# Performance work log

Hardware: AMD Instinct MI355X
Metric: run time of the kernel (lower is better)

Reference implementation:

```python
import jax, jax.numpy as jnp
import numpy as np

D_MODEL = 1024
NUM_HEADS = 16
D_K = D_MODEL // NUM_HEADS  # 64
THETA = 10000.0
B, S = 2, 2048


def _rope(x, cos, sin):
    # x: [b, h, s, d]; cos/sin: [s, d//2] (broadcast over b, h)
    x1 = x[..., 0::2]
    x2 = x[..., 1::2]
    y1 = x1 * cos - x2 * sin
    y2 = x1 * sin + x2 * cos
    # interleave back: stack on last dim then flatten pairs
    return jnp.stack([y1, y2], axis=-1).reshape(x.shape)


def setup_inputs() -> dict:
    key = jax.random.key(0)
    ks = jax.random.split(key, 5)
    scale = 1.0 / np.sqrt(D_MODEL)
    return {
        "x": jax.random.normal(ks[0], (B, S, D_MODEL), dtype=jnp.float32),
        "token_positions": jnp.arange(S, dtype=jnp.int32),
        "Wq": jax.random.normal(ks[1], (D_MODEL, D_MODEL), dtype=jnp.float32) * scale,
        "Wk": jax.random.normal(ks[2], (D_MODEL, D_MODEL), dtype=jnp.float32) * scale,
        "Wv": jax.random.normal(ks[3], (D_MODEL, D_MODEL), dtype=jnp.float32) * scale,
        "Wo": jax.random.normal(ks[4], (D_MODEL, D_MODEL), dtype=jnp.float32) * scale,
    }


def reference(x, token_positions, Wq, Wk, Wv, Wo):
    b, s, _ = x.shape
    # torch nn.Linear semantics (no bias in this repo's Linear): y = x @ W.T
    q = jnp.einsum("bsd,od->bso", x, Wq)
    k = jnp.einsum("bsd,od->bso", x, Wk)
    v = jnp.einsum("bsd,od->bso", x, Wv)
    # split heads: b s (h d) -> b h s d
    def split(t):
        return t.reshape(b, s, NUM_HEADS, D_K).transpose(0, 2, 1, 3)
    q, k, v = split(q), split(k), split(v)

    # RoPE tables
    inv_freq = 1.0 / (THETA ** (jnp.arange(0, D_K, 2, dtype=jnp.float32) / D_K))  # [d/2]
    freqs = token_positions.astype(jnp.float32)[:, None] * inv_freq[None, :]      # [s, d/2]
    cos, sin = jnp.cos(freqs), jnp.sin(freqs)
    q = _rope(q, cos, sin)
    k = _rope(k, cos, sin)

    scale = D_K ** (-0.5)
    scores = jnp.einsum("bhqd,bhkd->bhqk", q, k) * scale  # [b,h,s,s]
    causal = jnp.tril(jnp.ones((s, s), dtype=bool))
    scores = jnp.where(causal, scores, -jnp.inf)
    attn = jax.nn.softmax(scores, axis=-1)
    out = jnp.einsum("bhqk,bhkd->bhqd", attn, v)
    out = out.transpose(0, 2, 1, 3).reshape(b, s, D_MODEL)  # b h s d -> b s (h d)
    return jnp.einsum("bsd,od->bso", out, Wo)
```

## Files before the change

kernel.cpp:

```cpp
#include <hip/hip_runtime.h>
#include <hip/hip_bf16.h>
#include <math.h>

#define SS 2048

typedef __attribute__((ext_vector_type(8))) __bf16 bf16x8;
typedef __attribute__((ext_vector_type(4))) float f32x4;
typedef __attribute__((ext_vector_type(16))) float f32x16;
typedef __attribute__((ext_vector_type(4))) unsigned int u32x4;
typedef __attribute__((ext_vector_type(4))) unsigned short u16x4;

__device__ __forceinline__ f32x4 mfma16(bf16x8 a, bf16x8 b, f32x4 c) {
  return __builtin_amdgcn_mfma_f32_16x16x32_bf16(a, b, c, 0, 0, 0);
}
__device__ __forceinline__ f32x16 mfma32(bf16x8 a, bf16x8 b, f32x16 c) {
  return __builtin_amdgcn_mfma_f32_32x32x16_bf16(a, b, c, 0, 0, 0);
}

__device__ __forceinline__ void gld_lds16(const void* g, void* l) {
  __builtin_amdgcn_global_load_lds(
      (__attribute__((address_space(1))) void*)(g),
      (__attribute__((address_space(3))) void*)(l), 16, 0, 0);
}

#if __has_builtin(__builtin_amdgcn_exp2f)
#define EXP2F(x) __builtin_amdgcn_exp2f(x)
#else
#define EXP2F(x) __expf(0.69314718056f * (x))
#endif

__device__ __forceinline__ unsigned int cvtpk_bf16(float lo, float hi) {
  unsigned int r;
  asm("v_cvt_pk_bf16_f32 %0, %1, %2" : "=v"(r) : "v"(lo), "v"(hi));
  return r;
}
__device__ __forceinline__ void swap32(unsigned int& x, unsigned int& y) {
  asm("v_permlane32_swap_b32 %0, %1" : "+v"(x), "+v"(y));
}
__device__ __forceinline__ unsigned short bfu(float v) {
  __bf16 h = (__bf16)v;
  return __builtin_bit_cast(unsigned short, h);
}

__global__ void prep_kernel(const float* __restrict__ x, const float* __restrict__ Wq,
                            const float* __restrict__ Wk, const float* __restrict__ Wv,
                            const float* __restrict__ Wo, const int* __restrict__ pos,
                            __bf16* __restrict__ xb, __bf16* __restrict__ Wb,
                            float2* __restrict__ tab) {
  const int bid = blockIdx.x, tid = threadIdx.x;
  if (bid >= 4096) {
    int i = (bid - 4096) * 256 + tid;
    int s = i >> 5, j = i & 31;
    float p = (float)pos[s];
    float inv = exp2f((float)j * -0.41524101186098283f);
    float f = p * inv;
    float sn, cs;
    sincosf(f, &sn, &cs);
    tab[i] = make_float2(cs, sn);
    return;
  }
  const float* s;
  __bf16* d;
  size_t base;
  if (bid < 2048) { s = x; d = xb; base = bid; }
  else {
    int seg = (bid - 2048) >> 9;
    s = (seg == 0) ? Wq : (seg == 1) ? Wk : (seg == 2) ? Wv : Wo;
    d = Wb + (size_t)seg * 1024 * 1024;
    base = (bid - 2048) & 511;
  }
  size_t i = (base * 256 + tid) * 8;
  float4 a = *reinterpret_cast<const float4*>(s + i);
  float4 b = *reinterpret_cast<const float4*>(s + i + 4);
  bf16x8 o;
  o[0] = (__bf16)a.x; o[1] = (__bf16)a.y; o[2] = (__bf16)a.z; o[3] = (__bf16)a.w;
  o[4] = (__bf16)b.x; o[5] = (__bf16)b.y; o[6] = (__bf16)b.z; o[7] = (__bf16)b.w;
  *reinterpret_cast<bf16x8*>(d + i) = o;
}

__global__ __launch_bounds__(512, 1) void gemm256_kernel(
    const __bf16* __restrict__ A, const __bf16* __restrict__ Bw,
    __bf16* __restrict__ C, __bf16* __restrict__ Vt,
    const float2* __restrict__ tab) {
  const int K = 1024, N = 3072, nk = 32;
  __shared__ __align__(16) __bf16 sm[65536];
  __bf16* lsA = sm;
  __bf16* lsB = sm + 32768;

  const int tid = threadIdx.x;
  const int lane = tid & 63;
  const int wave = tid >> 6;
  const int wr = wave >> 2, wc = wave & 3;

  const int xcd = blockIdx.x & 7;
  const int ii = blockIdx.x >> 3;
  const int m0 = (2 * xcd + (ii & 1)) * 256;
  const int n0 = (ii >> 1) * 256;

  const f32x4 fzero = {0.f, 0.f, 0.f, 0.f};
  f32x4 acc[8][4];
#pragma unroll
  for (int f = 0; f < 8; ++f)
#pragma unroll
    for (int g = 0; g < 4; ++g) acc[f][g] = fzero;

  const int srow = tid >> 2, schunk = tid & 3;
  const int ssc = schunk ^ ((srow >> 1) & 3);
  const __bf16* gA = A + (size_t)(m0 + srow) * K + ssc * 8;
  const __bf16* gB = Bw + (size_t)(n0 + srow) * K + ssc * 8;
  const size_t half128 = (size_t)128 * K;

#define STAGE256(kt_)                                              \
  do {                                                             \
    const int kc_ = (kt_) & 3;                                     \
    const __bf16* ga_ = gA + (size_t)(kt_) * 32;                   \
    const __bf16* gb_ = gB + (size_t)(kt_) * 32;                   \
    gld_lds16(ga_, lsA + kc_ * 8192 + tid * 8);                    \
    gld_lds16(ga_ + half128, lsA + kc_ * 8192 + 4096 + tid * 8);   \
    gld_lds16(gb_, lsB + kc_ * 8192 + tid * 8);                    \
    gld_lds16(gb_ + half128, lsB + kc_ * 8192 + 4096 + tid * 8);   \
  } while (0)

  STAGE256(0);
  STAGE256(1);

  const int lrow = lane & 15, hi = lane >> 4;

#pragma unroll 1
  for (int kt = 0; kt < nk; ++kt) {
    const int ks = (kt & 3) * 8192;
    if (kt + 2 < nk) {
      STAGE256(kt + 2);
      asm volatile("s_waitcnt vmcnt(8)" ::: "memory");
    } else if (kt == nk - 2) {
      asm volatile("s_waitcnt vmcnt(4)" ::: "memory");
    } else {
      asm volatile("s_waitcnt vmcnt(0)" ::: "memory");
    }
    __builtin_amdgcn_s_barrier();

    bf16x8 bfr[4];
#pragma unroll
    for (int g = 0; g < 4; ++g) {
      const int r = wc * 64 + g * 16 + lrow;
      bfr[g] = *reinterpret_cast<const bf16x8*>(
          lsB + ks + r * 32 + ((hi ^ ((r >> 1) & 3)) * 8));
    }
    bf16x8 af[4];
#pragma unroll
    for (int f = 0; f < 4; ++f) {
      const int r = wr * 128 + f * 16 + lrow;
      af[f] = *reinterpret_cast<const bf16x8*>(
          lsA + ks + r * 32 + ((hi ^ ((r >> 1) & 3)) * 8));
    }
    __builtin_amdgcn_s_setprio(1);
#pragma unroll
    for (int f = 0; f < 4; ++f)
#pragma unroll
      for (int g = 0; g < 4; ++g) acc[f][g] = mfma16(af[f], bfr[g], acc[f][g]);
    __builtin_amdgcn_s_setprio(0);
#pragma unroll
    for (int f = 0; f < 4; ++f) {
      const int r = wr * 128 + (f + 4) * 16 + lrow;
      af[f] = *reinterpret_cast<const bf16x8*>(
          lsA + ks + r * 32 + ((hi ^ ((r >> 1) & 3)) * 8));
    }
    __builtin_amdgcn_s_setprio(1);
#pragma unroll
    for (int f = 0; f < 4; ++f)
#pragma unroll
      for (int g = 0; g < 4; ++g) acc[f + 4][g] = mfma16(af[f], bfr[g], acc[f + 4][g]);
    __builtin_amdgcn_s_setprio(0);
  }
#undef STAGE256

  const int crow = (lane >> 4) * 4, ccol = lane & 15;
  if (n0 < 2048) {
    const int par = ccol & 1;
#pragma unroll
    for (int f = 0; f < 8; ++f) {
#pragma unroll
      for (int t = 0; t < 4; ++t) {
        const int r = m0 + wr * 128 + f * 16 + crow + t;
        const int s = r & (SS - 1);
#pragma unroll
        for (int g = 0; g < 4; ++g) {
          const int c = n0 + wc * 64 + g * 16 + ccol;
          const int jj = (c >> 1) & 31;
          float2 cs = tab[(s << 5) | jj];
          float v = acc[f][g][t];
          float o = __shfl_xor(v, 1);
          float y = par ? fmaf(o, cs.y, v * cs.x) : fmaf(v, cs.x, -o * cs.y);
          C[(size_t)r * N + c] = (__bf16)y;
        }
      }
    }
  } else {
#pragma unroll
    for (int f = 0; f < 8; ++f) {
      const int r0 = m0 + wr * 128 + f * 16 + crow;
      const int bb = r0 >> 11, s0 = r0 & (SS - 1);
#pragma unroll
      for (int g = 0; g < 4; ++g) {
        const int c = n0 - 2048 + wc * 64 + g * 16 + ccol;
        const int hh = c >> 6, dd = c & 63;
        u16x4 pk;
#pragma unroll
        for (int t = 0; t < 4; ++t) pk[t] = bfu(acc[f][g][t]);
        *reinterpret_cast<u16x4*>(Vt + ((size_t)(bb * 16 + hh) * 64 + dd) * SS + s0) = pk;
      }
    }
  }
}

template <typename OutT>
__global__ __launch_bounds__(256) void gemm_bt_kernel(
    const __bf16* __restrict__ A, const __bf16* __restrict__ Bw,
    OutT* __restrict__ C, int MT, int N, int K) {
  __shared__ __align__(16) __bf16 lA[2][128 * 32];
  __shared__ __align__(16) __bf16 lB[2][128 * 32];
  const int tid = threadIdx.x;
  const int lane = tid & 63;
  const int wave = tid >> 6;
  const int wr = wave >> 1, wc = wave & 1;

  const int cpx = (int)gridDim.x >> 3;
  const int flat = blockIdx.x;
  const int wg = (flat & 7) * cpx + (flat >> 3);
  const int MB = MT >> 3;
  const int NT = (int)gridDim.x / MT;
  const int band = wg / (MB * NT);
  const int inner = wg % (MB * NT);
  const int m0 = (band * MB + (inner % MB)) * 128;
  const int n0 = (inner / MB) * 128;

  const f32x4 fzero = {0.f, 0.f, 0.f, 0.f};
  f32x4 acc[4][4];
#pragma unroll
  for (int i = 0; i < 4; ++i)
#pragma unroll
    for (int j = 0; j < 4; ++j) acc[i][j] = fzero;

  const int srow = tid >> 2, scol = (tid & 3) * 8;
  const __bf16* gA = A + (size_t)(m0 + srow) * K + scol;
  const __bf16* gB = Bw + (size_t)(n0 + srow) * K + scol;
  const size_t half = (size_t)64 * K;
  const int lrow = lane & 15, lk8 = (lane >> 4) * 8;

  gld_lds16(gA, &lA[0][tid * 8]);
  gld_lds16(gA + half, &lA[0][tid * 8 + 2048]);
  gld_lds16(gB, &lB[0][tid * 8]);
  gld_lds16(gB + half, &lB[0][tid * 8 + 2048]);
  __syncthreads();

  const int nk = K >> 5;
  for (int t = 0; t < nk; ++t) {
    const int buf = t & 1;
    if (t + 1 < nk) {
      const int kt = (t + 1) * 32;
      gld_lds16(gA + kt, &lA[buf ^ 1][tid * 8]);
      gld_lds16(gA + kt + half, &lA[buf ^ 1][tid * 8 + 2048]);
      gld_lds16(gB + kt, &lB[buf ^ 1][tid * 8]);
      gld_lds16(gB + kt + half, &lB[buf ^ 1][tid * 8 + 2048]);
    }
    bf16x8 af[4], bfr[4];
#pragma unroll
    for (int i = 0; i < 4; ++i)
      af[i] = *reinterpret_cast<const bf16x8*>(&lA[buf][(wr * 64 + i * 16 + lrow) * 32 + lk8]);
#pragma unroll
    for (int j = 0; j < 4; ++j)
      bfr[j] = *reinterpret_cast<const bf16x8*>(&lB[buf][(wc * 64 + j * 16 + lrow) * 32 + lk8]);
    __builtin_amdgcn_s_setprio(1);
#pragma unroll
    for (int i = 0; i < 4; ++i)
#pragma unroll
      for (int j = 0; j < 4; ++j) acc[i][j] = mfma16(af[i], bfr[j], acc[i][j]);
    __builtin_amdgcn_s_setprio(0);
    __syncthreads();
  }

  const int crow = (lane >> 4) * 4, ccol = lane & 15;
#pragma unroll
  for (int i = 0; i < 4; ++i) {
#pragma unroll
    for (int j = 0; j < 4; ++j) {
      int r = m0 + wr * 64 + i * 16 + crow;
      int c = n0 + wc * 64 + j * 16 + ccol;
#pragma unroll
      for (int t = 0; t < 4; ++t) C[(size_t)(r + t) * N + c] = (OutT)acc[i][j][t];
    }
  }
}

#define CEXP 0.18033688011112042f
#define SHIFT_B 16.0f

#define EXPSUM(S0, S1, L)                                                   \
  {                                                                         \
    float a0_ = 0.f, a1_ = 0.f, a2_ = 0.f, a3_ = 0.f;                       \
    _Pragma("unroll") for (int r = 0; r < 16; r += 4) {                     \
      S0[r] = EXP2F(fmaf(S0[r], CEXP, -SHIFT_B)); a0_ += S0[r];             \
      S0[r + 1] = EXP2F(fmaf(S0[r + 1], CEXP, -SHIFT_B)); a1_ += S0[r + 1]; \
      S0[r + 2] = EXP2F(fmaf(S0[r + 2], CEXP, -SHIFT_B)); a2_ += S0[r + 2]; \
      S0[r + 3] = EXP2F(fmaf(S0[r + 3], CEXP, -SHIFT_B)); a3_ += S0[r + 3]; \
    }                                                                       \
    _Pragma("unroll") for (int r = 0; r < 16; r += 4) {                     \
      S1[r] = EXP2F(fmaf(S1[r], CEXP, -SHIFT_B)); a0_ += S1[r];             \
      S1[r + 1] = EXP2F(fmaf(S1[r + 1], CEXP, -SHIFT_B)); a1_ += S1[r + 1]; \
      S1[r + 2] = EXP2F(fmaf(S1[r + 2], CEXP, -SHIFT_B)); a2_ += S1[r + 2]; \
      S1[r + 3] = EXP2F(fmaf(S1[r + 3], CEXP, -SHIFT_B)); a3_ += S1[r + 3]; \
    }                                                                       \
    float rs_ = (a0_ + a1_) + (a2_ + a3_);                                  \
    rs_ += __shfl_xor(rs_, 32);                                             \
    L += rs_;                                                               \
  }

__global__ __launch_bounds__(128) void attn_kernel(const __bf16* __restrict__ qkv,
                                                   const __bf16* __restrict__ Vt,
                                                   __bf16* __restrict__ AO) {
  const int bid = blockIdx.x;
  const int x = bid & 7, t7 = bid >> 3;
  const int low = t7 & 7, phi = (t7 >> 3) & 3, g = t7 >> 5;
  const int p = phi * 8 + x;
  const int b = p >> 4, h = p & 15;
  const int qt = (g == 0) ? low : (g == 1) ? 31 - low : (g == 2) ? 15 - low : 16 + low;

  const int tid = threadIdx.x;
  const int wave = tid >> 6, lane = tid & 63;
  const int q32 = lane & 31, hi = lane >> 5;
  const int qw0 = qt * 64 + wave * 32;
  const int q = qw0 + q32;

  __shared__ __align__(16) __bf16 smem[16384];
  __bf16* lK0 = smem;
  __bf16* lV0 = smem + 8192;

  bf16x8 qb[4];
  {
    const __bf16* qr = qkv + (size_t)(b * SS + q) * 3072 + h * 64;
#pragma unroll
    for (int slot = 0; slot < 4; ++slot)
      qb[slot] = *reinterpret_cast<const bf16x8*>(qr + slot * 16 + hi * 8);
  }

  const __bf16* kbase = qkv + (size_t)(b * SS) * 3072 + 1024 + h * 64;
  const __bf16* vbase = Vt + (size_t)((b * 16 + h) * 64) * SS;

  const int srow = tid >> 3, scg = tid & 7;
  const int ssc = 8 * (scg ^ (srow & 7));
  const __bf16* kG0 = kbase + (size_t)srow * 3072 + ssc;
  const __bf16* vG0 = vbase + (size_t)srow * SS + ssc;

#define STAGE(buf_, kt_)                                                      \
  do {                                                                        \
    const __bf16* kG = kG0 + (size_t)(kt_)*64 * 3072;                         \
    const __bf16* vG = vG0 + (size_t)(kt_)*64;                                \
    _Pragma("unroll") for (int u = 0; u < 4; ++u) {                           \
      gld_lds16(kG + (size_t)u * 16 * 3072, lK0 + (buf_)*4096 + tid * 8 + u * 1024); \
      gld_lds16(vG + (size_t)u * 16 * SS, lV0 + (buf_)*4096 + tid * 8 + u * 1024);   \
    }                                                                         \
  } while (0)

  f32x16 o0 = {0,0,0,0,0,0,0,0,0,0,0,0,0,0,0,0};
  f32x16 o1 = {0,0,0,0,0,0,0,0,0,0,0,0,0,0,0,0};
  float lsum = 0.f;

  const int nkt = qt + 1;
  STAGE(0, 0);
  __syncthreads();

  for (int kt = 0; kt < nkt; ++kt) {
    const int buf = kt & 1;
    const int kvb = kt * 64;
    if (kt + 1 < nkt) STAGE(buf ^ 1, kt + 1);

    const __bf16* lk = lK0 + buf * 4096;
    const __bf16* lv = lV0 + buf * 4096;

    f32x16 s0 = {0,0,0,0,0,0,0,0,0,0,0,0,0,0,0,0};
    f32x16 s1 = {0,0,0,0,0,0,0,0,0,0,0,0,0,0,0,0};
    __builtin_amdgcn_s_setprio(1);
#pragma unroll
    for (int slot = 0; slot < 4; ++slot) {
      const int swz = 8 * ((slot * 2 + hi) ^ (q32 & 7));
      bf16x8 k0 = *reinterpret_cast<const bf16x8*>(lk + q32 * 64 + swz);
      bf16x8 k1 = *reinterpret_cast<const bf16x8*>(lk + (32 + q32) * 64 + swz);
      s0 = mfma32(k0, qb[slot], s0);
      s1 = mfma32(k1, qb[slot], s1);
    }
    __builtin_amdgcn_s_setprio(0);

    if (kt == qt) {
#pragma unroll
      for (int r = 0; r < 16; ++r) {
        const int rowc = (r & 3) + 8 * (r >> 2) + 4 * hi;
        if (kvb + rowc > q) s0[r] = -INFINITY;
        if (kvb + 32 + rowc > q) s1[r] = -INFINITY;
      }
    }

    EXPSUM(s0, s1, lsum)

    bf16x8 pb[4];
    {
      unsigned int A = cvtpk_bf16(s0[0], s0[1]), B2 = cvtpk_bf16(s0[2], s0[3]);
      unsigned int C2 = cvtpk_bf16(s0[4], s0[5]), D2 = cvtpk_bf16(s0[6], s0[7]);
      swap32(A, C2); swap32(B2, D2);
      u32x4 t0 = {A, B2, C2, D2};
      pb[0] = __builtin_bit_cast(bf16x8, t0);
      unsigned int E = cvtpk_bf16(s0[8], s0[9]), F = cvtpk_bf16(s0[10], s0[11]);
      unsigned int G = cvtpk_bf16(s0[12], s0[13]), H = cvtpk_bf16(s0[14], s0[15]);
      swap32(E, G); swap32(F, H);
      u32x4 t1 = {E, F, G, H};
      pb[1] = __builtin_bit_cast(bf16x8, t1);
      unsigned int A3 = cvtpk_bf16(s1[0], s1[1]), B3 = cvtpk_bf16(s1[2], s1[3]);
      unsigned int C3 = cvtpk_bf16(s1[4], s1[5]), D3 = cvtpk_bf16(s1[6], s1[7]);
      swap32(A3, C3); swap32(B3, D3);
      u32x4 t2 = {A3, B3, C3, D3};
      pb[2] = __builtin_bit_cast(bf16x8, t2);
      unsigned int E3 = cvtpk_bf16(s1[8], s1[9]), F3 = cvtpk_bf16(s1[10], s1[11]);
      unsigned int G3 = cvtpk_bf16(s1[12], s1[13]), H3 = cvtpk_bf16(s1[14], s1[15]);
      swap32(E3, G3); swap32(F3, H3);
      u32x4 t3 = {E3, F3, G3, H3};
      pb[3] = __builtin_bit_cast(bf16x8, t3);
    }

    __builtin_amdgcn_s_setprio(1);
#pragma unroll
    for (int slot = 0; slot < 4; ++slot) {
      const int swz = 8 * ((slot * 2 + hi) ^ (q32 & 7));
      bf16x8 v0 = *reinterpret_cast<const bf16x8*>(lv + q32 * 64 + swz);
      bf16x8 v1 = *reinterpret_cast<const bf16x8*>(lv + (32 + q32) * 64 + swz);
      o0 = mfma32(v0, pb[slot], o0);
      o1 = mfma32(v1, pb[slot], o1);
    }
    __builtin_amdgcn_s_setprio(0);

    __syncthreads();
  }

  const float inv = 1.0f / lsum;
  __bf16* ol = smem + wave * 2304;
#pragma unroll
  for (int r = 0; r < 16; ++r) {
    const int d = (r & 3) + 8 * (r >> 2) + 4 * hi;
    ol[q32 * 72 + d] = (__bf16)(o0[r] * inv);
    ol[q32 * 72 + 32 + d] = (__bf16)(o1[r] * inv);
  }
#pragma unroll
  for (int pass = 0; pass < 4; ++pass) {
    const int idx = pass * 64 + lane;
    const int row = idx >> 3, colc = idx & 7;
    bf16x8 v = *reinterpret_cast<const bf16x8*>(ol + row * 72 + colc * 8);
    *reinterpret_cast<bf16x8*>(
        AO + (size_t)(b * SS + qt * 64 + wave * 32 + row) * 1024 + h * 64 + colc * 8) = v;
  }
#undef STAGE
}

extern "C" void kernel_launch(void* const* d_in, const int* in_sizes, int n_in,
                              void* d_out, int out_size, void* d_ws, size_t ws_size,
                              hipStream_t stream) {
  const float* x  = (const float*)d_in[0];
  const int* pos  = (const int*)d_in[1];
  const float* Wq = (const float*)d_in[2];
  const float* Wk = (const float*)d_in[3];
  const float* Wv = (const float*)d_in[4];
  const float* Wo = (const float*)d_in[5];

  __bf16* xb  = (__bf16*)d_ws;
  __bf16* Wb  = xb + (size_t)4096 * 1024;
  __bf16* qkv = Wb + (size_t)4096 * 1024;
  __bf16* Vt  = qkv + (size_t)4096 * 3072;
  __bf16* ao  = Vt + (size_t)2048 * 2048;
  float2* tab = (float2*)(ao + (size_t)4096 * 1024);

  prep_kernel<<<4352, 256, 0, stream>>>(x, Wq, Wk, Wv, Wo, pos, xb, Wb, tab);
  gemm256_kernel<<<192, 512, 0, stream>>>(xb, Wb, qkv, Vt, tab);
  attn_kernel<<<1024, 128, 0, stream>>>(qkv, Vt, ao);
  gemm_bt_kernel<float><<<256, 256, 0, stream>>>(
      ao, Wb + (size_t)3 * 1024 * 1024, (float*)d_out, 32, 1024, 1024);
}
```

Baseline: 113.5 us.

## Retile QKV GEMM to 256x192 for full CU coverage and rewrite output GEMM

The QKV projection GEMM now uses 256x192 tiles, so it launches 256 workgroups instead of 192 and fills all 256 CUs. Only six of the eight waves load the B tile, and the wait counts are adjusted per wave. The epilogue now decides per 16-column group whether to apply RoPE or write the transposed V. The output projection is replaced by a 512-thread kernel with a 4-stage swizzled LDS pipeline, XCD-aware tile mapping and a single barrier per k-step. The cost is a smaller N tile per workgroup, which lowers the compute per byte loaded.

```diff
diff --git a/kernel.cpp b/kernel.cpp
--- a/kernel.cpp
+++ b/kernel.cpp
@@ -83,7 +83,7 @@
     __bf16* __restrict__ C, __bf16* __restrict__ Vt,
     const float2* __restrict__ tab) {
   const int K = 1024, N = 3072, nk = 32;
-  __shared__ __align__(16) __bf16 sm[65536];
+  __shared__ __align__(16) __bf16 sm[57344];
   __bf16* lsA = sm;
   __bf16* lsB = sm + 32768;
 
@@ -91,34 +91,38 @@
   const int lane = tid & 63;
   const int wave = tid >> 6;
   const int wr = wave >> 2, wc = wave & 3;
+  const bool lowW = wave < 6;
 
   const int xcd = blockIdx.x & 7;
   const int ii = blockIdx.x >> 3;
   const int m0 = (2 * xcd + (ii & 1)) * 256;
-  const int n0 = (ii >> 1) * 256;
+  const int n0 = (ii >> 1) * 192;
 
   const f32x4 fzero = {0.f, 0.f, 0.f, 0.f};
-  f32x4 acc[8][4];
+  f32x4 acc[8][3];
 #pragma unroll
   for (int f = 0; f < 8; ++f)
 #pragma unroll
-    for (int g = 0; g < 4; ++g) acc[f][g] = fzero;
-
-  const int srow = tid >> 2, schunk = tid & 3;
-  const int ssc = schunk ^ ((srow >> 1) & 3);
-  const __bf16* gA = A + (size_t)(m0 + srow) * K + ssc * 8;
-  const __bf16* gB = Bw + (size_t)(n0 + srow) * K + ssc * 8;
-  const size_t half128 = (size_t)128 * K;
-
-#define STAGE256(kt_)                                              \
-  do {                                                             \
-    const int kc_ = (kt_) & 3;                                     \
-    const __bf16* ga_ = gA + (size_t)(kt_) * 32;                   \
-    const __bf16* gb_ = gB + (size_t)(kt_) * 32;                   \
-    gld_lds16(ga_, lsA + kc_ * 8192 + tid * 8);                    \
-    gld_lds16(ga_ + half128, lsA + kc_ * 8192 + 4096 + tid * 8);   \
-    gld_lds16(gb_, lsB + kc_ * 8192 + tid * 8);                    \
-    gld_lds16(gb_ + half128, lsB + kc_ * 8192 + 4096 + tid * 8);   \
+    for (int g = 0; g < 3; ++g) acc[f][g] = fzero;
+
+  const int arow0 = tid >> 2, ac = tid & 3;
+  const __bf16* gA0 = A + (size_t)(m0 + arow0) * K + 8 * (ac ^ ((arow0 >> 1) & 3));
+  const __bf16* gA1 = A + (size_t)(m0 + 128 + arow0) * K + 8 * (ac ^ (((arow0 + 128) >> 1) & 3));
+  const int bid0 = tid, bid1 = tid + 384;
+  const int br0 = bid0 >> 2, br1 = bid1 >> 2;
+  const __bf16* gB0 = Bw + (size_t)(n0 + br0) * K + 8 * ((bid0 & 3) ^ ((br0 >> 1) & 3));
+  const __bf16* gB1 = Bw + (size_t)(n0 + br1) * K + 8 * ((bid1 & 3) ^ ((br1 >> 1) & 3));
+
+#define STAGE256(kt_)                                                \
+  do {                                                               \
+    const int kc_ = (kt_) & 3;                                       \
+    const int ko_ = (kt_) * 32;                                      \
+    gld_lds16(gA0 + ko_, lsA + kc_ * 8192 + tid * 8);                \
+    gld_lds16(gA1 + ko_, lsA + kc_ * 8192 + 4096 + tid * 8);         \
+    if (lowW) {                                                      \
+      gld_lds16(gB0 + ko_, lsB + kc_ * 6144 + tid * 8);              \
+      gld_lds16(gB1 + ko_, lsB + kc_ * 6144 + 3072 + tid * 8);       \
+    }                                                                \
   } while (0)
 
   STAGE256(0);
@@ -128,82 +132,81 @@
 
 #pragma unroll 1
   for (int kt = 0; kt < nk; ++kt) {
-    const int ks = (kt & 3) * 8192;
+    const int ksA = (kt & 3) * 8192, ksB = (kt & 3) * 6144;
     if (kt + 2 < nk) {
       STAGE256(kt + 2);
-      asm volatile("s_waitcnt vmcnt(8)" ::: "memory");
+      if (lowW) asm volatile("s_waitcnt vmcnt(8)" ::: "memory");
+      else      asm volatile("s_waitcnt vmcnt(4)" ::: "memory");
     } else if (kt == nk - 2) {
-      asm volatile("s_waitcnt vmcnt(4)" ::: "memory");
+      if (lowW) asm volatile("s_waitcnt vmcnt(4)" ::: "memory");
+      else      asm volatile("s_waitcnt vmcnt(2)" ::: "memory");
     } else {
       asm volatile("s_waitcnt vmcnt(0)" ::: "memory");
     }
     __builtin_amdgcn_s_barrier();
 
-    bf16x8 bfr[4];
-#pragma unroll
-    for (int g = 0; g < 4; ++g) {
-      const int r = wc * 64 + g * 16 + lrow;
+    bf16x8 bfr[3];
+#pragma unroll
+    for (int g = 0; g < 3; ++g) {
+      const int r = wc * 48 + g * 16 + lrow;
       bfr[g] = *reinterpret_cast<const bf16x8*>(
-          lsB + ks + r * 32 + ((hi ^ ((r >> 1) & 3)) * 8));
+          lsB + ksB + r * 32 + ((hi ^ ((r >> 1) & 3)) * 8));
     }
     bf16x8 af[4];
 #pragma unroll
     for (int f = 0; f < 4; ++f) {
       const int r = wr * 128 + f * 16 + lrow;
       af[f] = *reinterpret_cast<const bf16x8*>(
-          lsA + ks + r * 32 + ((hi ^ ((r >> 1) & 3)) * 8));
+          lsA + ksA + r * 32 + ((hi ^ ((r >> 1) & 3)) * 8));
     }
     __builtin_amdgcn_s_setprio(1);
 #pragma unroll
     for (int f = 0; f < 4; ++f)
 #pragma unroll
-      for (int g = 0; g < 4; ++g) acc[f][g] = mfma16(af[f], bfr[g], acc[f][g]);
+      for (int g = 0; g < 3; ++g) acc[f][g] = mfma16(af[f], bfr[g], acc[f][g]);
     __builtin_amdgcn_s_setprio(0);
 #pragma unroll
     for (int f = 0; f < 4; ++f) {
       const int r = wr * 128 + (f + 4) * 16 + lrow;
       af[f] = *reinterpret_cast<const bf16x8*>(
-          lsA + ks + r * 32 + ((hi ^ ((r >> 1) & 3)) * 8));
+          lsA + ksA + r * 32 + ((hi ^ ((r >> 1) & 3)) * 8));
     }
     __builtin_amdgcn_s_setprio(1);
 #pragma unroll
     for (int f = 0; f < 4; ++f)
 #pragma unroll
-      for (int g = 0; g < 4; ++g) acc[f + 4][g] = mfma16(af[f], bfr[g], acc[f + 4][g]);
+      for (int g = 0; g < 3; ++g) acc[f + 4][g] = mfma16(af[f], bfr[g], acc[f + 4][g]);
     __builtin_amdgcn_s_setprio(0);
   }
 #undef STAGE256
 
   const int crow = (lane >> 4) * 4, ccol = lane & 15;
-  if (n0 < 2048) {
-    const int par = ccol & 1;
-#pragma unroll
-    for (int f = 0; f < 8; ++f) {
-#pragma unroll
-      for (int t = 0; t < 4; ++t) {
-        const int r = m0 + wr * 128 + f * 16 + crow + t;
-        const int s = r & (SS - 1);
-#pragma unroll
-        for (int g = 0; g < 4; ++g) {
-          const int c = n0 + wc * 64 + g * 16 + ccol;
-          const int jj = (c >> 1) & 31;
+  const int par = ccol & 1;
+#pragma unroll
+  for (int g = 0; g < 3; ++g) {
+    const int cb = n0 + wc * 48 + g * 16;
+    if (cb < 2048) {
+      const int jj = ((cb + ccol) >> 1) & 31;
+#pragma unroll
+      for (int f = 0; f < 8; ++f) {
+#pragma unroll
+        for (int t = 0; t < 4; ++t) {
+          const int r = m0 + wr * 128 + f * 16 + crow + t;
+          const int s = r & (SS - 1);
           float2 cs = tab[(s << 5) | jj];
           float v = acc[f][g][t];
           float o = __shfl_xor(v, 1);
           float y = par ? fmaf(o, cs.y, v * cs.x) : fmaf(v, cs.x, -o * cs.y);
-          C[(size_t)r * N + c] = (__bf16)y;
+          C[(size_t)r * N + cb + ccol] = (__bf16)y;
         }
       }
-    }
-  } else {
-#pragma unroll
-    for (int f = 0; f < 8; ++f) {
-      const int r0 = m0 + wr * 128 + f * 16 + crow;
-      const int bb = r0 >> 11, s0 = r0 & (SS - 1);
-#pragma unroll
-      for (int g = 0; g < 4; ++g) {
-        const int c = n0 - 2048 + wc * 64 + g * 16 + ccol;
-        const int hh = c >> 6, dd = c & 63;
+    } else {
+      const int c = cb - 2048 + ccol;
+      const int hh = c >> 6, dd = c & 63;
+#pragma unroll
+      for (int f = 0; f < 8; ++f) {
+        const int r0 = m0 + wr * 128 + f * 16 + crow;
+        const int bb = r0 >> 11, s0 = r0 & (SS - 1);
         u16x4 pk;
 #pragma unroll
         for (int t = 0; t < 4; ++t) pk[t] = bfu(acc[f][g][t]);
@@ -213,81 +216,92 @@
   }
 }
 
-template <typename OutT>
-__global__ __launch_bounds__(256) void gemm_bt_kernel(
+__global__ __launch_bounds__(512, 1) void gemm_out_kernel(
     const __bf16* __restrict__ A, const __bf16* __restrict__ Bw,
-    OutT* __restrict__ C, int MT, int N, int K) {
-  __shared__ __align__(16) __bf16 lA[2][128 * 32];
-  __shared__ __align__(16) __bf16 lB[2][128 * 32];
+    float* __restrict__ C) {
+  const int K = 1024, N = 1024, nk = 32;
+  __shared__ __align__(16) __bf16 sm[32768];
+  __bf16* lsA = sm;
+  __bf16* lsB = sm + 16384;
+
   const int tid = threadIdx.x;
   const int lane = tid & 63;
   const int wave = tid >> 6;
-  const int wr = wave >> 1, wc = wave & 1;
-
-  const int cpx = (int)gridDim.x >> 3;
-  const int flat = blockIdx.x;
-  const int wg = (flat & 7) * cpx + (flat >> 3);
-  const int MB = MT >> 3;
-  const int NT = (int)gridDim.x / MT;
-  const int band = wg / (MB * NT);
-  const int inner = wg % (MB * NT);
-  const int m0 = (band * MB + (inner % MB)) * 128;
-  const int n0 = (inner / MB) * 128;
+  const int wr = wave >> 2, wc = wave & 3;
+
+  const int xcd = blockIdx.x & 7;
+  const int ii = blockIdx.x >> 3;
+  const int m0 = (4 * xcd + (ii & 3)) * 128;
+  const int n0 = (ii >> 2) * 128;
 
   const f32x4 fzero = {0.f, 0.f, 0.f, 0.f};
-  f32x4 acc[4][4];
-#pragma unroll
-  for (int i = 0; i < 4; ++i)
-#pragma unroll
-    for (int j = 0; j < 4; ++j) acc[i][j] = fzero;
-
-  const int srow = tid >> 2, scol = (tid & 3) * 8;
-  const __bf16* gA = A + (size_t)(m0 + srow) * K + scol;
-  const __bf16* gB = Bw + (size_t)(n0 + srow) * K + scol;
-  const size_t half = (size_t)64 * K;
-  const int lrow = lane & 15, lk8 = (lane >> 4) * 8;
-
-  gld_lds16(gA, &lA[0][tid * 8]);
-  gld_lds16(gA + half, &lA[0][tid * 8 + 2048]);
-  gld_lds16(gB, &lB[0][tid * 8]);
-  gld_lds16(gB + half, &lB[0][tid * 8 + 2048]);
-  __syncthreads();
-
-  const int nk = K >> 5;
-  for (int t = 0; t < nk; ++t) {
-    const int buf = t & 1;
-    if (t + 1 < nk) {
-      const int kt = (t + 1) * 32;
-      gld_lds16(gA + kt, &lA[buf ^ 1][tid * 8]);
-      gld_lds16(gA + kt + half, &lA[buf ^ 1][tid * 8 + 2048]);
-      gld_lds16(gB + kt, &lB[buf ^ 1][tid * 8]);
-      gld_lds16(gB + kt + half, &lB[buf ^ 1][tid * 8 + 2048]);
-    }
-    bf16x8 af[4], bfr[4];
-#pragma unroll
-    for (int i = 0; i < 4; ++i)
-      af[i] = *reinterpret_cast<const bf16x8*>(&lA[buf][(wr * 64 + i * 16 + lrow) * 32 + lk8]);
-#pragma unroll
-    for (int j = 0; j < 4; ++j)
-      bfr[j] = *reinterpret_cast<const bf16x8*>(&lB[buf][(wc * 64 + j * 16 + lrow) * 32 + lk8]);
+  f32x4 acc[4][2];
+#pragma unroll
+  for (int f = 0; f < 4; ++f)
+#pragma unroll
+    for (int g = 0; g < 2; ++g) acc[f][g] = fzero;
+
+  const int srow = tid >> 2, sc = tid & 3;
+  const int ssc = 8 * (sc ^ ((srow >> 1) & 3));
+  const __bf16* gA = A + (size_t)(m0 + srow) * K + ssc;
+  const __bf16* gB = Bw + (size_t)(n0 + srow) * K + ssc;
+
+#define STAGEO(kt_)                                        \
+  do {                                                     \
+    const int kc_ = (kt_) & 3;                             \
+    gld_lds16(gA + (kt_) * 32, lsA + kc_ * 4096 + tid * 8);\
+    gld_lds16(gB + (kt_) * 32, lsB + kc_ * 4096 + tid * 8);\
+  } while (0)
+
+  STAGEO(0);
+  STAGEO(1);
+
+  const int lrow = lane & 15, hi = lane >> 4;
+
+#pragma unroll 1
+  for (int kt = 0; kt < nk; ++kt) {
+    const int ks = (kt & 3) * 4096;
+    if (kt + 2 < nk) {
+      STAGEO(kt + 2);
+      asm volatile("s_waitcnt vmcnt(4)" ::: "memory");
+    } else if (kt == nk - 2) {
+      asm volatile("s_waitcnt vmcnt(2)" ::: "memory");
+    } else {
+      asm volatile("s_waitcnt vmcnt(0)" ::: "memory");
+    }
+    __builtin_amdgcn_s_barrier();
+
+    bf16x8 bfr[2], af[4];
+#pragma unroll
+    for (int g = 0; g < 2; ++g) {
+      const int r = wc * 32 + g * 16 + lrow;
+      bfr[g] = *reinterpret_cast<const bf16x8*>(
+          lsB + ks + r * 32 + ((hi ^ ((r >> 1) & 3)) * 8));
+    }
+#pragma unroll
+    for (int f = 0; f < 4; ++f) {
+      const int r = wr * 64 + f * 16 + lrow;
+      af[f] = *reinterpret_cast<const bf16x8*>(
+          lsA + ks + r * 32 + ((hi ^ ((r >> 1) & 3)) * 8));
+    }
     __builtin_amdgcn_s_setprio(1);
 #pragma unroll
-    for (int i = 0; i < 4; ++i)
-#pragma unroll
-      for (int j = 0; j < 4; ++j) acc[i][j] = mfma16(af[i], bfr[j], acc[i][j]);
+    for (int f = 0; f < 4; ++f)
+#pragma unroll
+      for (int g = 0; g < 2; ++g) acc[f][g] = mfma16(af[f], bfr[g], acc[f][g]);
     __builtin_amdgcn_s_setprio(0);
-    __syncthreads();
-  }
+  }
+#undef STAGEO
 
   const int crow = (lane >> 4) * 4, ccol = lane & 15;
 #pragma unroll
-  for (int i = 0; i < 4; ++i) {
-#pragma unroll
-    for (int j = 0; j < 4; ++j) {
-      int r = m0 + wr * 64 + i * 16 + crow;
-      int c = n0 + wc * 64 + j * 16 + ccol;
-#pragma unroll
-      for (int t = 0; t < 4; ++t) C[(size_t)(r + t) * N + c] = (OutT)acc[i][j][t];
+  for (int f = 0; f < 4; ++f) {
+#pragma unroll
+    for (int g = 0; g < 2; ++g) {
+      int r = m0 + wr * 64 + f * 16 + crow;
+      int c = n0 + wc * 32 + g * 16 + ccol;
+#pragma unroll
+      for (int t = 0; t < 4; ++t) C[(size_t)(r + t) * N + c] = acc[f][g][t];
     }
   }
 }
@@ -476,8 +490,7 @@
   float2* tab = (float2*)(ao + (size_t)4096 * 1024);
 
   prep_kernel<<<4352, 256, 0, stream>>>(x, Wq, Wk, Wv, Wo, pos, xb, Wb, tab);
-  gemm256_kernel<<<192, 512, 0, stream>>>(xb, Wb, qkv, Vt, tab);
+  gemm256_kernel<<<256, 512, 0, stream>>>(xb, Wb, qkv, Vt, tab);
   attn_kernel<<<1024, 128, 0, stream>>>(qkv, Vt, ao);
-  gemm_bt_kernel<float><<<256, 256, 0, stream>>>(
-      ao, Wb + (size_t)3 * 1024 * 1024, (float*)d_out, 32, 1024, 1024);
-}
+  gemm_out_kernel<<<256, 512, 0, stream>>>(ao, Wb + (size_t)3 * 1024 * 1024, (float*)d_out);
+}
```

Result: faster. 101.6 us (-10.5%).
